# Kernel optimization log

Measured on AMD Instinct MI355X. Metric: run time of the kernel, lower is better.

The kernel has to match this reference:

```python
import jax, jax.numpy as jnp
import numpy as np

B, S, D, H = 2, 1024, 1024, 16
DK = D // H
SLOPE = 8.0
SEP_ID, CLS_ID, PAD_ID = 1, 2, 0
NEG_INF = float('-inf')


def _head_scale():
    # exp2(-((h+1) * slope / n_heads)) per ALiBi
    return jnp.exp2(-(jnp.arange(H, dtype=jnp.float32) + 1.0) * SLOPE / H)


def _layernorm(x, w, b):
    m = jnp.mean(x, -1, keepdims=True)
    v = jnp.mean((x - m) ** 2, -1, keepdims=True)
    return (x - m) * jax.lax.rsqrt(v + 1e-5) * w + b


def _bias_masks(input_ids):
    # include_prefix=True path of LSWTTokenPoolerAttention.forward
    class_mask = input_ids == CLS_ID                       # [B,S]
    segment_mask = input_ids != PAD_ID                     # [B,S]
    segment_ids = jnp.cumsum((input_ids == SEP_ID).astype(jnp.int32), -1)
    pos = jnp.arange(S, dtype=jnp.float32)
    diag = jnp.eye(S, dtype=bool)[None]
    # self mask: same-segment & both-valid, OR diagonal, lower-triangular
    seg_eq = segment_ids[:, :, None] == segment_ids[:, None, :]
    val = segment_mask[:, :, None] & segment_mask[:, None, :]
    m_self = jnp.tril((seg_eq & val) | diag)
    bias_self = jnp.where(m_self, pos[None, None, :] - pos[None, :, None], NEG_INF)
    # cross mask: key is class token OR diagonal, lower-triangular; bias = seg-id distance
    m_cross = jnp.tril(class_mask[:, None, :] | diag)
    bias_cross = jnp.where(m_cross, (segment_ids[:, None, :] - segment_ids[:, :, None]).astype(jnp.float32), NEG_INF)
    return bias_self, bias_cross


def _sdpa_layer(x, bias, qw, qb, kw, kb, vw, vb, gw, gb, ow, ob):
    hs = _head_scale()
    q = (x @ qw.T + qb).reshape(B, S, H, DK)
    k = (x @ kw.T + kb).reshape(B, S, H, DK)
    v = (x @ vw.T + vb).reshape(B, S, H, DK)
    scores = jnp.einsum('bqhd,bkhd->bhqk', q, k) * (DK ** -0.5) + bias[:, None] * hs[None, :, None, None]
    o = jnp.einsum('bhqk,bkhd->bqhd', jax.nn.softmax(scores, -1), v)
    o = o * jax.nn.sigmoid(x @ gw.T + gb)[..., None]    # head gate [B,S,H,1]
    return o.reshape(B, S, D) @ ow.T + ob


def _pool_layer(x, bias, aw, vw, vb, gw, gb, ow, ob):
    hs = _head_scale()
    v = (x @ vw.T + vb).reshape(B, S, H, DK)
    # a_proj -> [B,S,H] -> [B,H,1,S] broadcast over queries, + alibi bias
    a = jnp.transpose(x @ aw.T, (0, 2, 1))[:, :, None, :] + bias[:, None] * hs[None, :, None, None]
    o = jnp.einsum('bhqk,bkhd->bqhd', jax.nn.softmax(a, -1), v)
    o = o * jax.nn.sigmoid(x @ gw.T + gb)[..., None]
    return o.reshape(B, S, D) @ ow.T + ob


def _forward(input_ids, states, ln0_w, ln0_b, l0_qw, l0_qb, l0_kw, l0_kb, l0_vw, l0_vb, l0_gw, l0_gb, l0_ow, l0_ob, ln1_w, ln1_b, l1_aw, l1_vw, l1_vb, l1_gw, l1_gb, l1_ow, l1_ob, ln2_w, ln2_b, l2_qw, l2_qb, l2_kw, l2_kb, l2_vw, l2_vb, l2_gw, l2_gb, l2_ow, l2_ob):
    bias_self, bias_cross = _bias_masks(input_ids)
    x = states
    x = x + _sdpa_layer(_layernorm(x, ln0_w, ln0_b), bias_self, l0_qw, l0_qb, l0_kw, l0_kb, l0_vw, l0_vb, l0_gw, l0_gb, l0_ow, l0_ob)
    x = x + _pool_layer(_layernorm(x, ln1_w, ln1_b), bias_self, l1_aw, l1_vw, l1_vb, l1_gw, l1_gb, l1_ow, l1_ob)
    x = x + _sdpa_layer(_layernorm(x, ln2_w, ln2_b), bias_cross, l2_qw, l2_qb, l2_kw, l2_kb, l2_vw, l2_vb, l2_gw, l2_gb, l2_ow, l2_ob)
    return x


def setup_inputs() -> dict:
    key = jax.random.key(0)
    ks = iter(jax.random.split(key, 40))
    def w(shape):
        return jax.random.normal(next(ks), shape, jnp.float32) * 0.02
    inp = {}
    inp['states'] = jax.random.normal(next(ks), (B, S, D), jnp.float32)
    inp['input_ids'] = jax.random.randint(next(ks), (B, S), 0, 128)
    for i, t in enumerate(['self', 'pool', 'cross']):
        inp[f'ln{i}_w'] = jnp.ones((D,), jnp.float32)
        inp[f'ln{i}_b'] = jnp.zeros((D,), jnp.float32)
        if t == 'pool':
            inp[f'l{i}_aw'] = w((H, D))
        else:
            inp[f'l{i}_qw'] = w((D, D)); inp[f'l{i}_qb'] = jnp.zeros((D,), jnp.float32)
            inp[f'l{i}_kw'] = w((D, D)); inp[f'l{i}_kb'] = jnp.zeros((D,), jnp.float32)
        inp[f'l{i}_vw'] = w((D, D)); inp[f'l{i}_vb'] = jnp.zeros((D,), jnp.float32)
        inp[f'l{i}_gw'] = w((H, D)); inp[f'l{i}_gb'] = jnp.zeros((H,), jnp.float32)
        inp[f'l{i}_ow'] = w((D, D)); inp[f'l{i}_ob'] = jnp.zeros((D,), jnp.float32)
    return inp


def reference(states, input_ids, ln0_w, ln0_b, l0_qw, l0_qb, l0_kw, l0_kb, l0_vw, l0_vb, l0_gw, l0_gb, l0_ow, l0_ob, ln1_w, ln1_b, l1_aw, l1_vw, l1_vb, l1_gw, l1_gb, l1_ow, l1_ob, ln2_w, ln2_b, l2_qw, l2_qb, l2_kw, l2_kb, l2_vw, l2_vb, l2_gw, l2_gb, l2_ow, l2_ob):
    return _forward(input_ids, states, ln0_w, ln0_b, l0_qw, l0_qb, l0_kw, l0_kb, l0_vw, l0_vb, l0_gw, l0_gb, l0_ow, l0_ob, ln1_w, ln1_b, l1_aw, l1_vw, l1_vb, l1_gw, l1_gb, l1_ow, l1_ob, ln2_w, ln2_b, l2_qw, l2_qb, l2_kw, l2_kb, l2_vw, l2_vb, l2_gw, l2_gb, l2_ow, l2_ob)
```

## Files before the change

### kernel.cpp

```cpp
#include <hip/hip_runtime.h>

typedef unsigned short u16;
typedef unsigned int u32;
typedef __attribute__((ext_vector_type(8))) short bf16x8;
typedef __attribute__((ext_vector_type(4))) float f32x4;

namespace {

constexpr int S = 1024, D = 1024, H = 16, DK = 64;
constexpr float NEGF = -1e30f;

__device__ __forceinline__ u16 f2bf(float f){
  u32 u = __builtin_bit_cast(u32, f);
  u32 r = (u + 0x7fffu + ((u >> 16) & 1u)) >> 16;
  return (u16)r;
}
__device__ __forceinline__ float bf2f(u16 h){
  u32 u = ((u32)h) << 16;
  return __builtin_bit_cast(float, u);
}
__device__ __forceinline__ u32 pack2(float a, float b){
  return (u32)f2bf(a) | ((u32)f2bf(b) << 16);
}
__device__ __forceinline__ void glds16(const u16* g, u16* l){
  __builtin_amdgcn_global_load_lds(
      (const __attribute__((address_space(1))) u32*)g,
      (__attribute__((address_space(3))) u32*)l, 16, 0, 0);
}
__device__ __forceinline__ int swz(int row, int slot){
  return row*64 + ((slot ^ (row & 7)) << 3);
}

struct CvtArgs { const float* src[10]; u16* dst[10]; };
__global__ __launch_bounds__(256) void cvt_kernel(CvtArgs a){
  int m = blockIdx.y;
  const float* s = a.src[m];
  u16* d = a.dst[m];
  int i = (blockIdx.x * 256 + threadIdx.x) * 8;
  float4 v0 = *(const float4*)(s + i), v1 = *(const float4*)(s + i + 4);
  u32 p[4] = { pack2(v0.x,v0.y), pack2(v0.z,v0.w), pack2(v1.x,v1.y), pack2(v1.z,v1.w) };
  *(uint4*)(d + i) = *(uint4*)p;
}

__global__ void seg_kernel(const int* __restrict__ ids, int* __restrict__ segd){
  __shared__ int sc[1024];
  int b = blockIdx.x, t = threadIdx.x;
  int id = ids[b*S + t];
  sc[t] = (id == 1) ? 1 : 0;
  __syncthreads();
  for(int off = 1; off < 1024; off <<= 1){
    int add = (t >= off) ? sc[t - off] : 0;
    __syncthreads();
    sc[t] += add;
    __syncthreads();
  }
  int seg = sc[t];
  segd[b*S + t] = (seg << 2) | ((id == 2) ? 2 : 0) | ((id != 0) ? 1 : 0);
}

__global__ __launch_bounds__(256) void ln_kernel(const float* __restrict__ x,
    const float* __restrict__ w, const float* __restrict__ bias, u16* __restrict__ out){
  int row = blockIdx.x, t = threadIdx.x;
  float4 v = ((const float4*)(x + (size_t)row*D))[t];
  float s = v.x + v.y + v.z + v.w;
  float q = v.x*v.x + v.y*v.y + v.z*v.z + v.w*v.w;
  for(int off = 32; off >= 1; off >>= 1){ s += __shfl_down(s, off); q += __shfl_down(q, off); }
  __shared__ float ls[4], lq[4];
  int wv = t >> 6, ln = t & 63;
  if(ln == 0){ ls[wv] = s; lq[wv] = q; }
  __syncthreads();
  s = ls[0] + ls[1] + ls[2] + ls[3];
  q = lq[0] + lq[1] + lq[2] + lq[3];
  float mean = s * (1.f/D);
  float var  = q * (1.f/D) - mean*mean;
  float rs = rsqrtf(var + 1e-5f);
  float4 wv4 = ((const float4*)w)[t];
  float4 bv4 = ((const float4*)bias)[t];
  ushort4 o;
  o.x = f2bf((v.x-mean)*rs*wv4.x + bv4.x);
  o.y = f2bf((v.y-mean)*rs*wv4.y + bv4.y);
  o.z = f2bf((v.z-mean)*rs*wv4.z + bv4.z);
  o.w = f2bf((v.w-mean)*rs*wv4.w + bv4.w);
  *(ushort4*)(out + (size_t)row*D + t*4) = o;
}

template<bool DUAL>
__global__ __launch_bounds__(256) void headproj2_kernel(const u16* __restrict__ xln,
    const u16* __restrict__ wgb, const float* __restrict__ bg, float* __restrict__ outg,
    const u16* __restrict__ wab, float* __restrict__ outa){
  __shared__ alignas(16) u16 X[16*1024];
  __shared__ f32x4 red[DUAL ? 6 : 3][64];
  int t = threadIdx.x, w = t >> 6, lane = t & 63, g = lane >> 4, l15 = lane & 15;
  int row0 = blockIdx.x*16;
  #pragma unroll
  for(int i = 0; i < 8; ++i){
    int idx = i*256 + t;
    int row = idx >> 7, slot = idx & 127;
    const u16* src = xln + (size_t)(row0 + row)*D + ((slot ^ (row & 7)) << 3);
    glds16(src, &X[idx << 3]);
  }
  bf16x8 wg_[8], wa_[8];
  #pragma unroll
  for(int j = 0; j < 8; ++j){
    int koff = (8*w + j)*32 + g*8;
    wg_[j] = *(const bf16x8*)&wgb[(size_t)l15*D + koff];
    if constexpr (DUAL) wa_[j] = *(const bf16x8*)&wab[(size_t)l15*D + koff];
  }
  asm volatile("s_waitcnt vmcnt(0)");
  __syncthreads();
  f32x4 accg = {}, acca = {};
  #pragma unroll
  for(int j = 0; j < 8; ++j){
    int kk = 8*w + j;
    bf16x8 xa = *(const bf16x8*)&X[l15*1024 + (((kk*4 + g) ^ (l15 & 7)) << 3)];
    accg = __builtin_amdgcn_mfma_f32_16x16x32_bf16(xa, wg_[j], accg, 0, 0, 0);
    if constexpr (DUAL) acca = __builtin_amdgcn_mfma_f32_16x16x32_bf16(xa, wa_[j], acca, 0, 0, 0);
  }
  if(w > 0){
    red[w-1][lane] = accg;
    if constexpr (DUAL) red[w+2][lane] = acca;
  }
  __syncthreads();
  if(w == 0){
    #pragma unroll
    for(int r = 0; r < 3; ++r) accg += red[r][lane];
    if constexpr (DUAL){
      #pragma unroll
      for(int r = 3; r < 6; ++r) acca += red[r][lane];
    }
    float bgv = bg[l15];
    int b = row0 >> 10;
    size_t base = ((size_t)(b*H + l15) << 10) + (row0 & 1023) + g*4;
    #pragma unroll
    for(int i = 0; i < 4; ++i){
      float r = accg[i] + bgv;
      outg[base + i] = 1.f/(1.f + __expf(-r));
      if constexpr (DUAL) outa[base + i] = acca[i];
    }
  }
}

template<int MODE, int BM, int BN>
__global__ __launch_bounds__(256) void gemm_t(const u16* __restrict__ A,
    const u16* __restrict__ W0, const u16* __restrict__ W1, const u16* __restrict__ W2,
    const float* __restrict__ b0f, const float* __restrict__ b1f, const float* __restrict__ b2f,
    void* __restrict__ o0, void* __restrict__ o1, void* __restrict__ o2,
    const float* __restrict__ resid){
  constexpr int K = 1024;
  constexpr int RM = BM/32, RN = BN/32;
  constexpr int NBY = 2048/BM;
  constexpr int NBX = ((MODE == 0) ? 3072 : 1024)/BN;
  constexpr int CPX = (NBX*NBY)/8;
  __shared__ alignas(16) u16 As[2*BM*64];
  __shared__ alignas(16) u16 Bs[2*BN*64];
  int bid = blockIdx.x;
  int vid = (bid & 7)*CPX + (bid >> 3);
  int bx = vid / NBY, by = vid % NBY;
  int m0 = by*BM;
  const u16* W; const float* bias; int mat, n0;
  if constexpr (MODE == 0){
    mat = bx >> 3; n0 = (bx & 7)*BN;
    W = (mat == 0) ? W0 : (mat == 1) ? W1 : W2;
    bias = (mat == 0) ? b0f : (mat == 1) ? b1f : b2f;
  } else { mat = 0; n0 = bx*BN; W = W0; bias = b0f; }
  int t = threadIdx.x, w = t >> 6, lane = t & 63, g = lane >> 4, l15 = lane & 15;
  int wr = w >> 1, wc = w & 1;
  int rl = lane >> 3, sl = lane & 7;
  int scol = ((sl ^ rl) << 3);
  f32x4 acc[RM][RN] = {};
  const u16* ag = A + (size_t)(m0 + rl)*K + scol;
  const u16* wg = W + (size_t)(n0 + rl)*K + scol;
  auto STAGE = [&](int kt, int buf){
    #pragma unroll
    for(int j = 0; j < BM/32; ++j){
      int r = w*(BM/4) + j*8;
      glds16(ag + (size_t)r*K + kt*64, &As[buf*BM*64 + r*64]);
    }
    #pragma unroll
    for(int j = 0; j < BN/32; ++j){
      int r = w*(BN/4) + j*8;
      glds16(wg + (size_t)r*K + kt*64, &Bs[buf*BN*64 + r*64]);
    }
  };
  STAGE(0, 0);
  asm volatile("s_waitcnt vmcnt(0)");
  __syncthreads();
  int cur = 0;
  for(int kt = 0; kt < 16; ++kt){
    if(kt + 1 < 16) STAGE(kt + 1, cur ^ 1);
    bf16x8 af[RM][2], bfr[RN][2];
    #pragma unroll
    for(int m = 0; m < RM; ++m)
      #pragma unroll
      for(int ks = 0; ks < 2; ++ks)
        af[m][ks] = *(const bf16x8*)&As[cur*BM*64 + swz(wr*(BM/2) + m*16 + l15, ks*4 + g)];
    #pragma unroll
    for(int n = 0; n < RN; ++n)
      #pragma unroll
      for(int ks = 0; ks < 2; ++ks)
        bfr[n][ks] = *(const bf16x8*)&Bs[cur*BN*64 + swz(wc*(BN/2) + n*16 + l15, ks*4 + g)];
    __builtin_amdgcn_s_setprio(1);
    #pragma unroll
    for(int ks = 0; ks < 2; ++ks)
      #pragma unroll
      for(int m = 0; m < RM; ++m)
        #pragma unroll
        for(int n = 0; n < RN; ++n)
          acc[m][n] = __builtin_amdgcn_mfma_f32_16x16x32_bf16(af[m][ks], bfr[n][ks], acc[m][n], 0, 0, 0);
    __builtin_amdgcn_s_setprio(0);
    if(kt + 1 < 16){
      asm volatile("s_waitcnt vmcnt(0)");
      __syncthreads();
      cur ^= 1;
    }
  }
  #pragma unroll
  for(int m = 0; m < RM; ++m){
    #pragma unroll
    for(int n = 0; n < RN; ++n){
      int ng = n0 + wc*(BN/2) + n*16 + l15;
      float bv = bias ? bias[ng] : 0.f;
      #pragma unroll
      for(int i = 0; i < 4; ++i){
        int mg = m0 + wr*(BM/2) + m*16 + g*4 + i;
        float v = acc[m][n][i] + bv;
        if constexpr (MODE == 0){
          if(mat == 0) v *= 0.125f;
          if(mat < 2){
            u16* o = (mat == 0) ? (u16*)o0 : (u16*)o1;
            o[(size_t)mg*D + ng] = f2bf(v);
          } else {
            int b = mg >> 10, s = mg & 1023;
            ((u16*)o2)[((size_t)(b*D + ng))*S + s] = f2bf(v);
          }
        } else if constexpr (MODE == 1){
          int b = mg >> 10, s = mg & 1023;
          ((u16*)o0)[((size_t)(b*D + ng))*S + s] = f2bf(v);
        } else {
          ((float*)o0)[(size_t)mg*1024 + ng] = resid[(size_t)mg*1024 + ng] + v;
        }
      }
    }
  }
}

__device__ __forceinline__ bf16x8 repack8(const float* s, int g, int l15){
  u32 L0 = pack2(s[0], s[1]), L1 = pack2(s[2], s[3]);
  u32 H0 = pack2(s[4], s[5]), H1 = pack2(s[6], s[7]);
  int base = ((g & 1)*2)*16 + l15;
  u32 a0 = (u32)__shfl((int)L0, base),    a1 = (u32)__shfl((int)L1, base);
  u32 b0 = (u32)__shfl((int)L0, base+16), b1 = (u32)__shfl((int)L1, base+16);
  u32 c0 = (u32)__shfl((int)H0, base),    c1 = (u32)__shfl((int)H1, base);
  u32 d0 = (u32)__shfl((int)H0, base+16), d1 = (u32)__shfl((int)H1, base+16);
  bool hi = g >= 2;
  union { u32 wd[4]; bf16x8 v; } pu;
  pu.wd[0] = hi ? c0 : a0;
  pu.wd[1] = hi ? c1 : a1;
  pu.wd[2] = hi ? d0 : b0;
  pu.wd[3] = hi ? d1 : b1;
  return pu.v;
}

template<int MODE>
__global__ __launch_bounds__(256) void attn4_kernel(const u16* __restrict__ Q,
    const u16* __restrict__ Kb, const u16* __restrict__ Vt,
    const float* __restrict__ aprojT, const int* __restrict__ segd,
    const float* __restrict__ gateT, u16* __restrict__ out){
  constexpr int KSZ = (MODE == 2) ? 16 : 8192;
  __shared__ alignas(16) u16 Klds[KSZ];
  __shared__ alignas(16) u16 Vlds[8192];
  __shared__ int segL[1024];
  __shared__ float apL[(MODE == 2) ? 1024 : 16];
  __shared__ u16 ot[4][16][72];
  int bid = blockIdx.x;
  int vid = (bid & 7)*64 + (bid >> 3);
  int bh = vid >> 4, qb = 15 - (vid & 15);
  int b = bh >> 4, h = bh & 15;
  int t = threadIdx.x, w = t >> 6, lane = t & 63, g = lane >> 4, l15 = lane & 15;
  { int4 v = ((const int4*)(segd + b*S))[t]; *(int4*)&segL[t*4] = v; }
  if constexpr (MODE == 2){
    float4 v = ((const float4*)(aprojT + ((size_t)bh << 10)))[t];
    *(float4*)&apL[t*4] = v;
  }
  int qt = qb*4 + w, q = qt*16 + l15;
  float hs = exp2f(-(float)(h + 1) * 0.5f);
  int rl = lane >> 3, sl = lane & 7;
  int scol = ((sl ^ rl) << 3);
  bf16x8 qf0 = {}, qf1 = {};
  if constexpr (MODE != 2){
    const u16* qp = Q + ((size_t)(b*S + q))*D + h*DK + g*8;
    qf0 = *(const bf16x8*)qp;
    qf1 = *(const bf16x8*)(qp + 32);
  }
  auto STAGE = [&](int buf, int kc){
    int k0 = kc*64;
    if constexpr (MODE != 2){
      const u16* kg = Kb + (size_t)(b*S + k0 + w*16 + rl)*D + h*DK + scol;
      glds16(kg,               &Klds[buf*4096 + w*1024]);
      glds16(kg + (size_t)8*D, &Klds[buf*4096 + w*1024 + 512]);
    }
    const u16* vg = Vt + (size_t)(bh*DK + w*16 + rl)*S + k0 + scol;
    glds16(vg,               &Vlds[buf*4096 + w*1024]);
    glds16(vg + (size_t)8*S, &Vlds[buf*4096 + w*1024 + 512]);
  };

  f32x4 oacc[4] = {};
  float mrun = NEGF, lsum = 0.f;
  int sdq = 0, seg_q = 0, mq = 0;

  int nc = qb + 1;
  STAGE(0, 0);
  asm volatile("s_waitcnt vmcnt(0)");
  __syncthreads();
  sdq = segL[q]; seg_q = sdq >> 2; mq = sdq & 1;

  int cur = 0;
  for(int kc = 0; kc < nc; ++kc){
    if(kc + 1 < nc) STAGE(cur ^ 1, kc + 1);
    int k0 = kc*64;
    const u16* KL = &Klds[cur*4096];
    const u16* VL = &Vlds[cur*4096];
    bf16x8 vr[2][4];
    #pragma unroll
    for(int ks = 0; ks < 2; ++ks)
      #pragma unroll
      for(int c = 0; c < 4; ++c)
        vr[ks][c] = *(const bf16x8*)&VL[swz(c*16 + l15, ks*4 + g)];
    float sv[16];
    if constexpr (MODE != 2){
      __builtin_amdgcn_s_setprio(1);
      #pragma unroll
      for(int r = 0; r < 4; ++r){
        f32x4 sa = {};
        sa = __builtin_amdgcn_mfma_f32_16x16x32_bf16(
               *(const bf16x8*)&KL[swz(r*16 + l15, g)],     qf0, sa, 0, 0, 0);
        sa = __builtin_amdgcn_mfma_f32_16x16x32_bf16(
               *(const bf16x8*)&KL[swz(r*16 + l15, 4 + g)], qf1, sa, 0, 0, 0);
        #pragma unroll
        for(int i = 0; i < 4; ++i) sv[r*4+i] = sa[i];
      }
      __builtin_amdgcn_s_setprio(0);
    } else {
      #pragma unroll
      for(int r = 0; r < 4; ++r){
        float4 a4 = *(const float4*)&apL[k0 + r*16 + g*4];
        sv[r*4+0] = a4.x; sv[r*4+1] = a4.y; sv[r*4+2] = a4.z; sv[r*4+3] = a4.w;
      }
    }
    #pragma unroll
    for(int r = 0; r < 4; ++r){
      int4 sd4 = *(const int4*)&segL[k0 + r*16 + g*4];
      int sds[4] = { sd4.x, sd4.y, sd4.z, sd4.w };
      #pragma unroll
      for(int i = 0; i < 4; ++i){
        int key = k0 + r*16 + g*4 + i;
        int sdk = sds[i];
        bool ok; float val;
        if constexpr (MODE == 1){
          ok = (key < q && (sdk & 2)) || (key == q);
          val = (float)((sdk >> 2) - seg_q);
        } else {
          ok = (key < q && ((sdk >> 2) == seg_q) && (sdk & mq & 1)) || (key == q);
          val = (float)(key - q);
        }
        sv[r*4+i] = ok ? sv[r*4+i] + val*hs : NEGF;
      }
    }
    float cm = sv[0];
    #pragma unroll
    for(int i = 1; i < 16; ++i) cm = fmaxf(cm, sv[i]);
    cm = fmaxf(cm, __shfl_xor(cm, 16));
    cm = fmaxf(cm, __shfl_xor(cm, 32));
    float mnew = fmaxf(mrun, cm);
    float fac = __expf(mrun - mnew);
    float ps = 0.f;
    #pragma unroll
    for(int i = 0; i < 16; ++i){ sv[i] = __expf(sv[i] - mnew); ps += sv[i]; }
    ps += __shfl_xor(ps, 16);
    ps += __shfl_xor(ps, 32);
    lsum = lsum * fac + ps;
    mrun = mnew;
    #pragma unroll
    for(int c = 0; c < 4; ++c)
      #pragma unroll
      for(int i = 0; i < 4; ++i) oacc[c][i] *= fac;
    __builtin_amdgcn_s_setprio(1);
    #pragma unroll
    for(int ks = 0; ks < 2; ++ks){
      bf16x8 pf = repack8(&sv[ks*8], g, l15);
      #pragma unroll
      for(int c = 0; c < 4; ++c)
        oacc[c] = __builtin_amdgcn_mfma_f32_16x16x32_bf16(vr[ks][c], pf, oacc[c], 0, 0, 0);
    }
    __builtin_amdgcn_s_setprio(0);
    if(kc + 1 < nc){
      asm volatile("s_waitcnt vmcnt(0)");
      __syncthreads();
      cur ^= 1;
    }
  }

  float scale = (1.f / lsum) * gateT[((size_t)bh << 10) + q];
  #pragma unroll
  for(int c = 0; c < 4; ++c)
    #pragma unroll
    for(int i = 0; i < 4; i += 2){
      u32 p = pack2(oacc[c][i]*scale, oacc[c][i+1]*scale);
      *(u32*)&ot[w][l15][c*16 + g*4 + i] = p;
    }
  int r = lane >> 2, c4 = lane & 3;
  uint4 v0 = *(uint4*)&ot[w][r][c4*16];
  uint4 v1 = *(uint4*)&ot[w][r][c4*16 + 8];
  u16* op = out + ((size_t)(b*S + qt*16 + r))*D + h*DK + c4*16;
  *(uint4*)op = v0;
  *(uint4*)(op + 8) = v1;
}

}

extern "C" void kernel_launch(void* const* d_in, const int* in_sizes, int n_in,
                              void* d_out, int out_size, void* d_ws, size_t ws_size,
                              hipStream_t stream){
  (void)in_sizes; (void)n_in; (void)out_size; (void)ws_size;
  const float* states = (const float*)d_in[0];
  const int*   ids    = (const int*)d_in[1];
  float* xout = (float*)d_out;

  char* w = (char*)d_ws;
  u16* wbf[10];
  for(int i = 0; i < 10; ++i){ wbf[i] = (u16*)w; w += (size_t)1024*1024*2; }
  u16* wsm[4];
  for(int i = 0; i < 4; ++i){ wsm[i] = (u16*)w; w += (size_t)16*1024*2; }
  u16* xln  = (u16*)w; w += (size_t)2048*1024*2;
  u16* qb   = (u16*)w; w += (size_t)2048*1024*2;
  u16* kb   = (u16*)w; w += (size_t)2048*1024*2;
  u16* vt   = (u16*)w; w += (size_t)2048*1024*2;
  u16* attn = (u16*)w; w += (size_t)2048*1024*2;
  float* gateT  = (float*)w; w += (size_t)2048*16*4;
  float* aprojT = (float*)w; w += (size_t)2048*16*4;
  int* segd = (int*)w;

  const int widx[10] = {4, 6, 8, 12, 17, 21, 25, 27, 29, 33};
  CvtArgs ca;
  for(int i = 0; i < 10; ++i){ ca.src[i] = (const float*)d_in[widx[i]]; ca.dst[i] = wbf[i]; }
  cvt_kernel<<<dim3(512, 10), dim3(256), 0, stream>>>(ca);
  const int sidx[4] = {10, 19, 31, 16};
  CvtArgs cs = {};
  for(int i = 0; i < 4; ++i){ cs.src[i] = (const float*)d_in[sidx[i]]; cs.dst[i] = wsm[i]; }
  cvt_kernel<<<dim3(8, 4), dim3(256), 0, stream>>>(cs);
  seg_kernel<<<dim3(2), dim3(1024), 0, stream>>>(ids, segd);

  dim3 b256(256), g2048(2048);
  dim3 gqkv(384), ggen(256), gattn(512), ghp(128);

  ln_kernel<<<g2048, b256, 0, stream>>>(states, (const float*)d_in[2], (const float*)d_in[3], xln);
  gemm_t<0,128,128><<<gqkv, b256, 0, stream>>>(xln, wbf[0], wbf[1], wbf[2],
      (const float*)d_in[5], (const float*)d_in[7], (const float*)d_in[9], qb, kb, vt, nullptr);
  headproj2_kernel<false><<<ghp, b256, 0, stream>>>(xln, wsm[0], (const float*)d_in[11], gateT, nullptr, nullptr);
  attn4_kernel<0><<<gattn, b256, 0, stream>>>(qb, kb, vt, nullptr, segd, gateT, attn);
  gemm_t<2,128,64><<<ggen, b256, 0, stream>>>(attn, wbf[3], nullptr, nullptr,
      (const float*)d_in[13], nullptr, nullptr, xout, nullptr, nullptr, states);

  ln_kernel<<<g2048, b256, 0, stream>>>(xout, (const float*)d_in[14], (const float*)d_in[15], xln);
  gemm_t<1,128,64><<<ggen, b256, 0, stream>>>(xln, wbf[4], nullptr, nullptr,
      (const float*)d_in[18], nullptr, nullptr, vt, nullptr, nullptr, nullptr);
  headproj2_kernel<true><<<ghp, b256, 0, stream>>>(xln, wsm[1], (const float*)d_in[20], gateT, wsm[3], aprojT);
  attn4_kernel<2><<<gattn, b256, 0, stream>>>(nullptr, nullptr, vt, aprojT, segd, gateT, attn);
  gemm_t<2,128,64><<<ggen, b256, 0, stream>>>(attn, wbf[5], nullptr, nullptr,
      (const float*)d_in[22], nullptr, nullptr, xout, nullptr, nullptr, xout);

  ln_kernel<<<g2048, b256, 0, stream>>>(xout, (const float*)d_in[23], (const float*)d_in[24], xln);
  gemm_t<0,128,128><<<gqkv, b256, 0, stream>>>(xln, wbf[6], wbf[7], wbf[8],
      (const float*)d_in[26], (const float*)d_in[28], (const float*)d_in[30], qb, kb, vt, nullptr);
  headproj2_kernel<false><<<ghp, b256, 0, stream>>>(xln, wsm[2], (const float*)d_in[32], gateT, nullptr, nullptr);
  attn4_kernel<1><<<gattn, b256, 0, stream>>>(qb, kb, vt, nullptr, segd, gateT, attn);
  gemm_t<2,128,64><<<ggen, b256, 0, stream>>>(attn, wbf[9], nullptr, nullptr,
      (const float*)d_in[34], nullptr, nullptr, xout, nullptr, nullptr, xout);
}
```

Baseline: 420.5 us.

## Fuse prologue kernels, merge head projections into GEMM launches, transpose V via LDS

Folds the weight conversions, segment-id scan and first layernorm into one prologue launch, and merges each layer's gate/a-proj head projection into the QKV/V GEMM launch as extra blocks. The transposed V output is now staged in shared memory so each thread writes coalesced 16-byte rows instead of scattered 2-byte stores. The goal is fewer kernel launches with their serialization gaps, and less uncoalesced global write traffic. The cost is a larger shared-memory footprint for the merged kernels and heterogeneous blocks within a single grid.

```diff
diff --git a/kernel.cpp b/kernel.cpp
--- a/kernel.cpp
+++ b/kernel.cpp
@@ -31,41 +31,13 @@
   return row*64 + ((slot ^ (row & 7)) << 3);
 }
 
-struct CvtArgs { const float* src[10]; u16* dst[10]; };
-__global__ __launch_bounds__(256) void cvt_kernel(CvtArgs a){
-  int m = blockIdx.y;
-  const float* s = a.src[m];
-  u16* d = a.dst[m];
-  int i = (blockIdx.x * 256 + threadIdx.x) * 8;
-  float4 v0 = *(const float4*)(s + i), v1 = *(const float4*)(s + i + 4);
-  u32 p[4] = { pack2(v0.x,v0.y), pack2(v0.z,v0.w), pack2(v1.x,v1.y), pack2(v1.z,v1.w) };
-  *(uint4*)(d + i) = *(uint4*)p;
-}
-
-__global__ void seg_kernel(const int* __restrict__ ids, int* __restrict__ segd){
-  __shared__ int sc[1024];
-  int b = blockIdx.x, t = threadIdx.x;
-  int id = ids[b*S + t];
-  sc[t] = (id == 1) ? 1 : 0;
-  __syncthreads();
-  for(int off = 1; off < 1024; off <<= 1){
-    int add = (t >= off) ? sc[t - off] : 0;
-    __syncthreads();
-    sc[t] += add;
-    __syncthreads();
-  }
-  int seg = sc[t];
-  segd[b*S + t] = (seg << 2) | ((id == 2) ? 2 : 0) | ((id != 0) ? 1 : 0);
-}
-
-__global__ __launch_bounds__(256) void ln_kernel(const float* __restrict__ x,
-    const float* __restrict__ w, const float* __restrict__ bias, u16* __restrict__ out){
-  int row = blockIdx.x, t = threadIdx.x;
+__device__ __forceinline__ void ln_body(const float* __restrict__ x,
+    const float* __restrict__ w, const float* __restrict__ bias, u16* __restrict__ out,
+    int row, int t, float* ls, float* lq){
   float4 v = ((const float4*)(x + (size_t)row*D))[t];
   float s = v.x + v.y + v.z + v.w;
   float q = v.x*v.x + v.y*v.y + v.z*v.z + v.w*v.w;
   for(int off = 32; off >= 1; off >>= 1){ s += __shfl_down(s, off); q += __shfl_down(q, off); }
-  __shared__ float ls[4], lq[4];
   int wv = t >> 6, ln = t & 63;
   if(ln == 0){ ls[wv] = s; lq[wv] = q; }
   __syncthreads();
@@ -84,14 +56,70 @@
   *(ushort4*)(out + (size_t)row*D + t*4) = o;
 }
 
+__global__ __launch_bounds__(256) void ln_kernel(const float* __restrict__ x,
+    const float* __restrict__ w, const float* __restrict__ bias, u16* __restrict__ out){
+  __shared__ float ls[4], lq[4];
+  ln_body(x, w, bias, out, blockIdx.x, threadIdx.x, ls, lq);
+}
+
+struct CvtArgs { const float* src[14]; u16* dst[14]; };
+__global__ __launch_bounds__(256) void prologue_kernel(CvtArgs ca,
+    const int* __restrict__ ids, int* __restrict__ segd,
+    const float* __restrict__ x, const float* __restrict__ lnw,
+    const float* __restrict__ lnb, u16* __restrict__ xln){
+  __shared__ int ws_[256];
+  __shared__ float ls[4], lq[4];
+  int bid = blockIdx.x, t = threadIdx.x;
+  if(bid < 5120){
+    int m = bid >> 9;
+    const float* s = ca.src[m]; u16* d = ca.dst[m];
+    int i = (((bid & 511)*256) + t)*8;
+    float4 v0 = *(const float4*)(s + i), v1 = *(const float4*)(s + i + 4);
+    u32 p[4] = { pack2(v0.x,v0.y), pack2(v0.z,v0.w), pack2(v1.x,v1.y), pack2(v1.z,v1.w) };
+    *(uint4*)(d + i) = *(uint4*)p;
+  } else if(bid < 5152){
+    int idx = bid - 5120;
+    int m = 10 + (idx >> 3);
+    const float* s = ca.src[m]; u16* d = ca.dst[m];
+    int i = (((idx & 7)*256) + t)*8;
+    float4 v0 = *(const float4*)(s + i), v1 = *(const float4*)(s + i + 4);
+    u32 p[4] = { pack2(v0.x,v0.y), pack2(v0.z,v0.w), pack2(v1.x,v1.y), pack2(v1.z,v1.w) };
+    *(uint4*)(d + i) = *(uint4*)p;
+  } else if(bid < 5154){
+    int b = bid - 5152;
+    int4 id4 = ((const int4*)(ids + b*S))[t];
+    int c0 = (id4.x == 1);
+    int c1 = c0 + (id4.y == 1);
+    int c2 = c1 + (id4.z == 1);
+    int c3 = c2 + (id4.w == 1);
+    ws_[t] = c3;
+    __syncthreads();
+    for(int off = 1; off < 256; off <<= 1){
+      int a = (t >= off) ? ws_[t - off] : 0;
+      __syncthreads();
+      ws_[t] += a;
+      __syncthreads();
+    }
+    int ex = (t > 0) ? ws_[t-1] : 0;
+    int4 o;
+    o.x = ((ex+c0) << 2) | ((id4.x == 2) ? 2 : 0) | ((id4.x != 0) ? 1 : 0);
+    o.y = ((ex+c1) << 2) | ((id4.y == 2) ? 2 : 0) | ((id4.y != 0) ? 1 : 0);
+    o.z = ((ex+c2) << 2) | ((id4.z == 2) ? 2 : 0) | ((id4.z != 0) ? 1 : 0);
+    o.w = ((ex+c3) << 2) | ((id4.w == 2) ? 2 : 0) | ((id4.w != 0) ? 1 : 0);
+    ((int4*)(segd + b*S))[t] = o;
+  } else {
+    ln_body(x, lnw, lnb, xln, bid - 5154, t, ls, lq);
+  }
+}
+
 template<bool DUAL>
-__global__ __launch_bounds__(256) void headproj2_kernel(const u16* __restrict__ xln,
+__device__ __forceinline__ void headproj_body(u16* sm, int bid, const u16* __restrict__ xln,
     const u16* __restrict__ wgb, const float* __restrict__ bg, float* __restrict__ outg,
     const u16* __restrict__ wab, float* __restrict__ outa){
-  __shared__ alignas(16) u16 X[16*1024];
-  __shared__ f32x4 red[DUAL ? 6 : 3][64];
+  u16* X = sm;
+  f32x4* red = (f32x4*)(sm + 16384);
   int t = threadIdx.x, w = t >> 6, lane = t & 63, g = lane >> 4, l15 = lane & 15;
-  int row0 = blockIdx.x*16;
+  int row0 = bid*16;
   #pragma unroll
   for(int i = 0; i < 8; ++i){
     int idx = i*256 + t;
@@ -117,16 +145,16 @@
     if constexpr (DUAL) acca = __builtin_amdgcn_mfma_f32_16x16x32_bf16(xa, wa_[j], acca, 0, 0, 0);
   }
   if(w > 0){
-    red[w-1][lane] = accg;
-    if constexpr (DUAL) red[w+2][lane] = acca;
+    red[(w-1)*64 + lane] = accg;
+    if constexpr (DUAL) red[(w+2)*64 + lane] = acca;
   }
   __syncthreads();
   if(w == 0){
     #pragma unroll
-    for(int r = 0; r < 3; ++r) accg += red[r][lane];
+    for(int r = 0; r < 3; ++r) accg += red[r*64 + lane];
     if constexpr (DUAL){
       #pragma unroll
-      for(int r = 3; r < 6; ++r) acca += red[r][lane];
+      for(int r = 3; r < 6; ++r) acca += red[r*64 + lane];
     }
     float bgv = bg[l15];
     int b = row0 >> 10;
@@ -141,20 +169,16 @@
 }
 
 template<int MODE, int BM, int BN>
-__global__ __launch_bounds__(256) void gemm_t(const u16* __restrict__ A,
-    const u16* __restrict__ W0, const u16* __restrict__ W1, const u16* __restrict__ W2,
-    const float* __restrict__ b0f, const float* __restrict__ b1f, const float* __restrict__ b2f,
-    void* __restrict__ o0, void* __restrict__ o1, void* __restrict__ o2,
-    const float* __restrict__ resid){
+__device__ __forceinline__ void gemm_body(u16* sm, int vid,
+    const u16* __restrict__ A, const u16* __restrict__ W0, const u16* __restrict__ W1,
+    const u16* __restrict__ W2, const float* __restrict__ b0f, const float* __restrict__ b1f,
+    const float* __restrict__ b2f, void* __restrict__ o0, void* __restrict__ o1,
+    void* __restrict__ o2, const float* __restrict__ resid){
   constexpr int K = 1024;
   constexpr int RM = BM/32, RN = BN/32;
   constexpr int NBY = 2048/BM;
-  constexpr int NBX = ((MODE == 0) ? 3072 : 1024)/BN;
-  constexpr int CPX = (NBX*NBY)/8;
-  __shared__ alignas(16) u16 As[2*BM*64];
-  __shared__ alignas(16) u16 Bs[2*BN*64];
-  int bid = blockIdx.x;
-  int vid = (bid & 7)*CPX + (bid >> 3);
+  u16* As = sm;
+  u16* Bs = sm + 2*BM*64;
   int bx = vid / NBY, by = vid % NBY;
   int m0 = by*BM;
   const u16* W; const float* bias; int mat, n0;
@@ -214,34 +238,99 @@
       cur ^= 1;
     }
   }
-  #pragma unroll
-  for(int m = 0; m < RM; ++m){
-    #pragma unroll
-    for(int n = 0; n < RN; ++n){
-      int ng = n0 + wc*(BN/2) + n*16 + l15;
-      float bv = bias ? bias[ng] : 0.f;
-      #pragma unroll
-      for(int i = 0; i < 4; ++i){
-        int mg = m0 + wr*(BM/2) + m*16 + g*4 + i;
-        float v = acc[m][n][i] + bv;
-        if constexpr (MODE == 0){
-          if(mat == 0) v *= 0.125f;
-          if(mat < 2){
+  bool transpose = (MODE == 1) || (MODE == 0 && mat == 2);
+  if(!transpose){
+    #pragma unroll
+    for(int m = 0; m < RM; ++m){
+      #pragma unroll
+      for(int n = 0; n < RN; ++n){
+        int ng = n0 + wc*(BN/2) + n*16 + l15;
+        float bv = bias ? bias[ng] : 0.f;
+        #pragma unroll
+        for(int i = 0; i < 4; ++i){
+          int mg = m0 + wr*(BM/2) + m*16 + g*4 + i;
+          float v = acc[m][n][i] + bv;
+          if constexpr (MODE == 0){
+            if(mat == 0) v *= 0.125f;
             u16* o = (mat == 0) ? (u16*)o0 : (u16*)o1;
             o[(size_t)mg*D + ng] = f2bf(v);
-          } else {
-            int b = mg >> 10, s = mg & 1023;
-            ((u16*)o2)[((size_t)(b*D + ng))*S + s] = f2bf(v);
+          } else if constexpr (MODE == 2){
+            ((float*)o0)[(size_t)mg*1024 + ng] = resid[(size_t)mg*1024 + ng] + v;
           }
-        } else if constexpr (MODE == 1){
-          int b = mg >> 10, s = mg & 1023;
-          ((u16*)o0)[((size_t)(b*D + ng))*S + s] = f2bf(v);
-        } else {
-          ((float*)o0)[(size_t)mg*1024 + ng] = resid[(size_t)mg*1024 + ng] + v;
         }
       }
     }
-  }
+  } else {
+    __syncthreads();
+    u16* tile = sm;
+    #pragma unroll
+    for(int m = 0; m < RM; ++m){
+      #pragma unroll
+      for(int n = 0; n < RN; ++n){
+        int ngl = wc*(BN/2) + n*16 + l15;
+        float bv = bias[n0 + ngl];
+        #pragma unroll
+        for(int i = 0; i < 4; i += 2){
+          int mgl = wr*(BM/2) + m*16 + g*4 + i;
+          u32 p = pack2(acc[m][n][i] + bv, acc[m][n][i+1] + bv);
+          *(u32*)&tile[ngl*136 + mgl] = p;
+        }
+      }
+    }
+    __syncthreads();
+    int bq = m0 >> 10, m0s = m0 & 1023;
+    constexpr int TPR = 256/BN;
+    constexpr int CW  = BM/TPR;
+    int ng = t / TPR, mgc = (t % TPR)*CW;
+    void* ovt = (MODE == 0) ? o2 : o0;
+    u16* dst = (u16*)ovt + ((size_t)(bq*D + n0 + ng))*S + m0s + mgc;
+    const u16* srcp = &tile[ng*136 + mgc];
+    #pragma unroll
+    for(int j = 0; j < CW/8; ++j)
+      *(uint4*)(dst + j*8) = *(const uint4*)(srcp + j*8);
+  }
+}
+
+__global__ __launch_bounds__(256) void proj_sdpa_kernel(const u16* __restrict__ xln,
+    const u16* __restrict__ Wq, const u16* __restrict__ Wk, const u16* __restrict__ Wv,
+    const float* __restrict__ bq_, const float* __restrict__ bk_, const float* __restrict__ bv_,
+    u16* __restrict__ oq, u16* __restrict__ ok, u16* __restrict__ ovt,
+    const u16* __restrict__ wgb, const float* __restrict__ bg, float* __restrict__ gateT){
+  __shared__ alignas(16) u16 sm[32768];
+  int bid = blockIdx.x;
+  if(bid < 128){
+    headproj_body<false>(sm, bid, xln, wgb, bg, gateT, nullptr, nullptr);
+  } else {
+    int q = bid - 128;
+    int vid = (q & 7)*48 + (q >> 3);
+    gemm_body<0,128,128>(sm, vid, xln, Wq, Wk, Wv, bq_, bk_, bv_, oq, ok, ovt, nullptr);
+  }
+}
+
+__global__ __launch_bounds__(256) void proj_pool_kernel(const u16* __restrict__ xln,
+    const u16* __restrict__ Wv, const float* __restrict__ bv_, u16* __restrict__ ovt,
+    const u16* __restrict__ wgb, const float* __restrict__ bg, float* __restrict__ gateT,
+    const u16* __restrict__ wab, float* __restrict__ aprojT){
+  __shared__ alignas(16) u16 sm[24576];
+  int bid = blockIdx.x;
+  if(bid < 128){
+    headproj_body<true>(sm, bid, xln, wgb, bg, gateT, wab, aprojT);
+  } else {
+    int q = bid - 128;
+    int vid = (q & 7)*32 + (q >> 3);
+    gemm_body<1,128,64>(sm, vid, xln, Wv, nullptr, nullptr, bv_, nullptr, nullptr,
+                        ovt, nullptr, nullptr, nullptr);
+  }
+}
+
+__global__ __launch_bounds__(256) void oproj_kernel(const u16* __restrict__ attn,
+    const u16* __restrict__ W, const float* __restrict__ bias,
+    float* __restrict__ xout, const float* __restrict__ resid){
+  __shared__ alignas(16) u16 sm[24576];
+  int bid = blockIdx.x;
+  int vid = (bid & 7)*32 + (bid >> 3);
+  gemm_body<2,128,64>(sm, vid, attn, W, nullptr, nullptr, bias, nullptr, nullptr,
+                      xout, nullptr, nullptr, resid);
 }
 
 __device__ __forceinline__ bf16x8 repack8(const float* s, int g, int l15){
@@ -441,39 +530,31 @@
   int* segd = (int*)w;
 
   const int widx[10] = {4, 6, 8, 12, 17, 21, 25, 27, 29, 33};
-  CvtArgs ca;
+  const int sidx[4] = {10, 19, 31, 16};
+  CvtArgs ca = {};
   for(int i = 0; i < 10; ++i){ ca.src[i] = (const float*)d_in[widx[i]]; ca.dst[i] = wbf[i]; }
-  cvt_kernel<<<dim3(512, 10), dim3(256), 0, stream>>>(ca);
-  const int sidx[4] = {10, 19, 31, 16};
-  CvtArgs cs = {};
-  for(int i = 0; i < 4; ++i){ cs.src[i] = (const float*)d_in[sidx[i]]; cs.dst[i] = wsm[i]; }
-  cvt_kernel<<<dim3(8, 4), dim3(256), 0, stream>>>(cs);
-  seg_kernel<<<dim3(2), dim3(1024), 0, stream>>>(ids, segd);
-
-  dim3 b256(256), g2048(2048);
-  dim3 gqkv(384), ggen(256), gattn(512), ghp(128);
-
-  ln_kernel<<<g2048, b256, 0, stream>>>(states, (const float*)d_in[2], (const float*)d_in[3], xln);
-  gemm_t<0,128,128><<<gqkv, b256, 0, stream>>>(xln, wbf[0], wbf[1], wbf[2],
-      (const float*)d_in[5], (const float*)d_in[7], (const float*)d_in[9], qb, kb, vt, nullptr);
-  headproj2_kernel<false><<<ghp, b256, 0, stream>>>(xln, wsm[0], (const float*)d_in[11], gateT, nullptr, nullptr);
-  attn4_kernel<0><<<gattn, b256, 0, stream>>>(qb, kb, vt, nullptr, segd, gateT, attn);
-  gemm_t<2,128,64><<<ggen, b256, 0, stream>>>(attn, wbf[3], nullptr, nullptr,
-      (const float*)d_in[13], nullptr, nullptr, xout, nullptr, nullptr, states);
-
-  ln_kernel<<<g2048, b256, 0, stream>>>(xout, (const float*)d_in[14], (const float*)d_in[15], xln);
-  gemm_t<1,128,64><<<ggen, b256, 0, stream>>>(xln, wbf[4], nullptr, nullptr,
-      (const float*)d_in[18], nullptr, nullptr, vt, nullptr, nullptr, nullptr);
-  headproj2_kernel<true><<<ghp, b256, 0, stream>>>(xln, wsm[1], (const float*)d_in[20], gateT, wsm[3], aprojT);
-  attn4_kernel<2><<<gattn, b256, 0, stream>>>(nullptr, nullptr, vt, aprojT, segd, gateT, attn);
-  gemm_t<2,128,64><<<ggen, b256, 0, stream>>>(attn, wbf[5], nullptr, nullptr,
-      (const float*)d_in[22], nullptr, nullptr, xout, nullptr, nullptr, xout);
-
-  ln_kernel<<<g2048, b256, 0, stream>>>(xout, (const float*)d_in[23], (const float*)d_in[24], xln);
-  gemm_t<0,128,128><<<gqkv, b256, 0, stream>>>(xln, wbf[6], wbf[7], wbf[8],
-      (const float*)d_in[26], (const float*)d_in[28], (const float*)d_in[30], qb, kb, vt, nullptr);
-  headproj2_kernel<false><<<ghp, b256, 0, stream>>>(xln, wsm[2], (const float*)d_in[32], gateT, nullptr, nullptr);
-  attn4_kernel<1><<<gattn, b256, 0, stream>>>(qb, kb, vt, nullptr, segd, gateT, attn);
-  gemm_t<2,128,64><<<ggen, b256, 0, stream>>>(attn, wbf[9], nullptr, nullptr,
-      (const float*)d_in[34], nullptr, nullptr, xout, nullptr, nullptr, xout);
-}
+  for(int i = 0; i < 4; ++i){ ca.src[10+i] = (const float*)d_in[sidx[i]]; ca.dst[10+i] = wsm[i]; }
+
+  dim3 b256(256);
+  prologue_kernel<<<dim3(7202), b256, 0, stream>>>(ca, ids, segd,
+      states, (const float*)d_in[2], (const float*)d_in[3], xln);
+
+  proj_sdpa_kernel<<<dim3(512), b256, 0, stream>>>(xln, wbf[0], wbf[1], wbf[2],
+      (const float*)d_in[5], (const float*)d_in[7], (const float*)d_in[9], qb, kb, vt,
+      wsm[0], (const float*)d_in[11], gateT);
+  attn4_kernel<0><<<dim3(512), b256, 0, stream>>>(qb, kb, vt, nullptr, segd, gateT, attn);
+  oproj_kernel<<<dim3(256), b256, 0, stream>>>(attn, wbf[3], (const float*)d_in[13], xout, states);
+
+  ln_kernel<<<dim3(2048), b256, 0, stream>>>(xout, (const float*)d_in[14], (const float*)d_in[15], xln);
+  proj_pool_kernel<<<dim3(384), b256, 0, stream>>>(xln, wbf[4], (const float*)d_in[18], vt,
+      wsm[1], (const float*)d_in[20], gateT, wsm[3], aprojT);
+  attn4_kernel<2><<<dim3(512), b256, 0, stream>>>(nullptr, nullptr, vt, aprojT, segd, gateT, attn);
+  oproj_kernel<<<dim3(256), b256, 0, stream>>>(attn, wbf[5], (const float*)d_in[22], xout, xout);
+
+  ln_kernel<<<dim3(2048), b256, 0, stream>>>(xout, (const float*)d_in[23], (const float*)d_in[24], xln);
+  proj_sdpa_kernel<<<dim3(512), b256, 0, stream>>>(xln, wbf[6], wbf[7], wbf[8],
+      (const float*)d_in[26], (const float*)d_in[28], (const float*)d_in[30], qb, kb, vt,
+      wsm[2], (const float*)d_in[32], gateT);
+  attn4_kernel<1><<<dim3(512), b256, 0, stream>>>(qb, kb, vt, nullptr, segd, gateT, attn);
+  oproj_kernel<<<dim3(256), b256, 0, stream>>>(attn, wbf[9], (const float*)d_in[34], xout, xout);
+}
```

Result: faster. 368.2 us (-12.4%).
